# Kernel optimization log

Measured on AMD Instinct MI355X. Metric: run time of the kernel, lower is better.

The kernel has to match this reference:

```python
import jax, jax.numpy as jnp
import numpy as np

N_NODES = 100000
N_EDGES = 600000
IN_C = 128


def setup_inputs() -> dict:
    key = jax.random.key(0)
    ks = jax.random.split(key, 10)
    x = jax.random.normal(ks[0], (N_NODES, IN_C), dtype=jnp.float32)
    edge_index = jax.random.randint(ks[1], (2, N_EDGES), 0, N_NODES, dtype=jnp.int64)
    edge_weight = jax.random.uniform(ks[2], (N_EDGES,), dtype=jnp.float32)
    s = 1.0 / np.sqrt(IN_C)
    # EvolveGCNO initial GCN weight [in, in]
    W0 = jax.random.uniform(ks[3], (IN_C, IN_C), minval=-s, maxval=s, dtype=jnp.float32)
    # GRU(input=in, hidden=in) params, gate order (r, z, n)
    W_ih = jax.random.uniform(ks[4], (3 * IN_C, IN_C), minval=-s, maxval=s, dtype=jnp.float32)
    W_hh = jax.random.uniform(ks[5], (3 * IN_C, IN_C), minval=-s, maxval=s, dtype=jnp.float32)
    b_ih = jax.random.uniform(ks[6], (3 * IN_C,), minval=-s, maxval=s, dtype=jnp.float32)
    b_hh = jax.random.uniform(ks[7], (3 * IN_C,), minval=-s, maxval=s, dtype=jnp.float32)
    cls_w = jax.random.uniform(ks[8], (1, IN_C), minval=-s, maxval=s, dtype=jnp.float32)
    cls_b = jax.random.uniform(ks[9], (1,), minval=-s, maxval=s, dtype=jnp.float32)
    return {"x": x, "edge_index": edge_index, "edge_weight": edge_weight,
            "W0": W0, "W_ih": W_ih, "W_hh": W_hh, "b_ih": b_ih, "b_hh": b_hh,
            "cls_w": cls_w, "cls_b": cls_b}


def reference(x, edge_index, edge_weight, W0, W_ih, W_hh, b_ih, b_hh, cls_w, cls_b):
    n = x.shape[0]
    # --- EvolveGCNO: GRU step with input = hidden = W0 (batch = in_channels rows) ---
    gi = W0 @ W_ih.T + b_ih
    gh = W0 @ W_hh.T + b_hh
    i_r, i_z, i_n = jnp.split(gi, 3, axis=1)
    h_r, h_z, h_n = jnp.split(gh, 3, axis=1)
    r = jax.nn.sigmoid(i_r + h_r)
    z = jax.nn.sigmoid(i_z + h_z)
    cand = jnp.tanh(i_n + r * h_n)
    W = (1.0 - z) * cand + z * W0  # evolved GCN weight [in, in]
    # --- GCNConv with fixed W: add self-loops, symmetric normalization ---
    loops = jnp.arange(n, dtype=edge_index.dtype)
    row = jnp.concatenate([edge_index[0], loops])  # source
    col = jnp.concatenate([edge_index[1], loops])  # target
    w = jnp.concatenate([edge_weight, jnp.ones((n,), x.dtype)])
    deg = jax.ops.segment_sum(w, col, num_segments=n)
    dinv = jnp.where(deg > 0, jax.lax.rsqrt(jnp.maximum(deg, 1e-30)), 0.0)
    norm = dinv[row] * w * dinv[col]  # [E+N]
    h = x @ W  # [N, in]
    agg = jax.ops.segment_sum(norm[:, None] * h[row], col, num_segments=n)  # [N, in]
    # --- ReLU + linear classifier ---
    h = jax.nn.relu(agg)
    return h @ cls_w.T + cls_b  # [N, 1]
```

## Files before the change

kernel.cpp:

```cpp
#include <hip/hip_runtime.h>
#include <math.h>

#define IN_C 128

typedef short short8 __attribute__((ext_vector_type(8)));
typedef float floatx4 __attribute__((ext_vector_type(4)));
typedef unsigned long long u64;

static __device__ __forceinline__ unsigned short f2bf(float f) {
    unsigned int u = __float_as_uint(f);
    u += 0x7fffu + ((u >> 16) & 1u);
    return (unsigned short)(u >> 16);
}

static __device__ __forceinline__ u64 pack_sn(unsigned int src, float norm) {
    return (u64)src | ((u64)__float_as_uint(norm) << 32);
}

__global__ __launch_bounds__(256) void evolve_hist(
        const float* __restrict__ W0, const float* __restrict__ Wih,
        const float* __restrict__ Whh, const float* __restrict__ bih,
        const float* __restrict__ bhh, unsigned short* __restrict__ Wbt,
        const int* __restrict__ coli, const float* __restrict__ ew,
        u64* __restrict__ pk, unsigned int* __restrict__ rank, int E) {
    const int b = blockIdx.x;
    const int t = threadIdx.x;

    if (b < 64) {
        __shared__ float w0row[2][IN_C];
        const int r2 = t >> 7;
        const int j = t & 127;
        const int i = b * 2 + r2;
        w0row[r2][j] = W0[i * IN_C + j];
        __syncthreads();
        float ir = bih[j], iz = bih[j + IN_C], inn = bih[j + 2 * IN_C];
        float hr = bhh[j], hz = bhh[j + IN_C], hnn = bhh[j + 2 * IN_C];
        const float* wr = &Wih[(size_t)j * IN_C];
        const float* wz = &Wih[(size_t)(j + IN_C) * IN_C];
        const float* wn = &Wih[(size_t)(j + 2 * IN_C) * IN_C];
        const float* ur = &Whh[(size_t)j * IN_C];
        const float* uz = &Whh[(size_t)(j + IN_C) * IN_C];
        const float* un = &Whh[(size_t)(j + 2 * IN_C) * IN_C];
        #pragma unroll 4
        for (int k = 0; k < IN_C; ++k) {
            const float a = w0row[r2][k];
            ir = fmaf(a, wr[k], ir); iz = fmaf(a, wz[k], iz); inn = fmaf(a, wn[k], inn);
            hr = fmaf(a, ur[k], hr); hz = fmaf(a, uz[k], hz); hnn = fmaf(a, un[k], hnn);
        }
        const float r = 1.0f / (1.0f + expf(-(ir + hr)));
        const float z = 1.0f / (1.0f + expf(-(iz + hz)));
        const float cand = tanhf(inn + r * hnn);
        Wbt[j * IN_C + i] = f2bf((1.0f - z) * cand + z * w0row[r2][j]);
    } else {
        const int e0 = ((b - 64) * 256 + t) * 4;
        if (e0 + 3 < E) {
            const int4 c4 = *(const int4*)&coli[e0];
            const float4 w4 = *(const float4*)&ew[e0];
            const u64 o0 = atomicAdd(&pk[c4.x], (1ull << 32) | (u64)(unsigned int)(w4.x * 16777216.0f));
            const u64 o1 = atomicAdd(&pk[c4.y], (1ull << 32) | (u64)(unsigned int)(w4.y * 16777216.0f));
            const u64 o2 = atomicAdd(&pk[c4.z], (1ull << 32) | (u64)(unsigned int)(w4.z * 16777216.0f));
            const u64 o3 = atomicAdd(&pk[c4.w], (1ull << 32) | (u64)(unsigned int)(w4.w * 16777216.0f));
            uint4 rk;
            rk.x = (unsigned int)(o0 >> 32); rk.y = (unsigned int)(o1 >> 32);
            rk.z = (unsigned int)(o2 >> 32); rk.w = (unsigned int)(o3 >> 32);
            *(uint4*)&rank[e0] = rk;
        } else {
            for (int e = e0; e < E; ++e) {
                const u64 o = atomicAdd(&pk[coli[e]],
                    (1ull << 32) | (u64)(unsigned int)(ew[e] * 16777216.0f));
                rank[e] = (unsigned int)(o >> 32);
            }
        }
    }
}

__global__ void scan1(const u64* __restrict__ pk, int* __restrict__ rowptr,
                      int* __restrict__ partials, float* __restrict__ dinv, int n) {
    __shared__ int s[256];
    const int t = threadIdx.x;
    const int i = blockIdx.x * 256 + t;
    const u64 pv = (i < n) ? pk[i] : 0ull;
    if (i < n)
        dinv[i] = rsqrtf((float)(unsigned int)(pv & 0xffffffffull) * (1.0f / 16777216.0f) + 1.0f);
    s[t] = (int)(pv >> 32);
    __syncthreads();
    #pragma unroll
    for (int off = 1; off < 256; off <<= 1) {
        const int v = (t >= off) ? s[t - off] : 0;
        __syncthreads();
        s[t] += v;
        __syncthreads();
    }
    if (i < n) rowptr[i] = (t == 0) ? 0 : s[t - 1];
    if (t == 255) partials[blockIdx.x] = s[255];
}

__global__ __launch_bounds__(512) void scan23(int* __restrict__ rowptr,
                                              const int* __restrict__ partials,
                                              int nb, int n, int E) {
    __shared__ int s[512];
    const int t = threadIdx.x;
    const int b = blockIdx.x;
    s[t] = (t < nb) ? partials[t] : 0;
    __syncthreads();
    #pragma unroll
    for (int off = 1; off < 512; off <<= 1) {
        const int v = (t >= off) ? s[t - off] : 0;
        __syncthreads();
        s[t] += v;
        __syncthreads();
    }
    const int add = (b == 0) ? 0 : s[b - 1];
    if (t < 256) {
        const int i = b * 256 + t;
        if (i < n) rowptr[i] += add;
    }
    if (b == 0 && t == 0) rowptr[n] = E;
}

#define ALD 136
__global__ __launch_bounds__(256) void place_gemm(
        const int* __restrict__ rowi, const int* __restrict__ coli,
        const float* __restrict__ ew, const float* __restrict__ dinv,
        const int* __restrict__ rowptr, const unsigned int* __restrict__ rank,
        u64* __restrict__ edge_sn, int E, int PB,
        const float* __restrict__ x, const unsigned short* __restrict__ Wbt,
        unsigned short* __restrict__ hb, int n) {
    __shared__ unsigned short As[128 * ALD];
    __shared__ unsigned short Ws[128 * ALD];
    const int b = blockIdx.x;
    const int t = threadIdx.x;

    if (b < PB) {
        const int e0 = (b * 256 + t) * 4;
        if (e0 + 3 < E) {
            const int4 r4 = *(const int4*)&rowi[e0];
            const int4 c4 = *(const int4*)&coli[e0];
            const float4 w4 = *(const float4*)&ew[e0];
            const uint4 rk = *(const uint4*)&rank[e0];
            __builtin_nontemporal_store(pack_sn((unsigned)r4.x, dinv[r4.x] * w4.x * dinv[c4.x]), &edge_sn[rowptr[c4.x] + rk.x]);
            __builtin_nontemporal_store(pack_sn((unsigned)r4.y, dinv[r4.y] * w4.y * dinv[c4.y]), &edge_sn[rowptr[c4.y] + rk.y]);
            __builtin_nontemporal_store(pack_sn((unsigned)r4.z, dinv[r4.z] * w4.z * dinv[c4.z]), &edge_sn[rowptr[c4.z] + rk.z]);
            __builtin_nontemporal_store(pack_sn((unsigned)r4.w, dinv[r4.w] * w4.w * dinv[c4.w]), &edge_sn[rowptr[c4.w] + rk.w]);
        } else {
            for (int e = e0; e < E; ++e) {
                const int r = rowi[e], c = coli[e];
                edge_sn[rowptr[c] + rank[e]] = pack_sn((unsigned)r, dinv[r] * ew[e] * dinv[c]);
            }
        }
        return;
    }

    const size_t row0 = (size_t)(b - PB) * 128;

    for (int idx = t; idx < 2048; idx += 256) {
        const int nn = idx >> 4, k8 = (idx & 15) * 8;
        *(uint4*)&Ws[nn * ALD + k8] = *(const uint4*)&Wbt[nn * IN_C + k8];
    }
    for (int idx = t; idx < 4096; idx += 256) {
        const int r = idx >> 5, c4 = (idx & 31) * 4;
        size_t row = row0 + r;
        if (row >= (size_t)n) row = (size_t)n - 1;
        const float4 v = *(const float4*)&x[row * IN_C + c4];
        ushort4 bb;
        bb.x = f2bf(v.x); bb.y = f2bf(v.y); bb.z = f2bf(v.z); bb.w = f2bf(v.w);
        *(ushort4*)&As[r * ALD + c4] = bb;
    }
    __syncthreads();

    const int w = t >> 6, lane = t & 63, ln = lane & 15, quad = lane >> 4;
    floatx4 acc[2][8];
    #pragma unroll
    for (int mt = 0; mt < 2; ++mt)
        #pragma unroll
        for (int nt = 0; nt < 8; ++nt)
            acc[mt][nt] = (floatx4){0.f, 0.f, 0.f, 0.f};

    #pragma unroll
    for (int k0 = 0; k0 < 128; k0 += 32) {
        const short8 a0 = *(const short8*)&As[(w * 32 + ln) * ALD + k0 + quad * 8];
        const short8 a1 = *(const short8*)&As[(w * 32 + 16 + ln) * ALD + k0 + quad * 8];
        #pragma unroll
        for (int nt = 0; nt < 8; ++nt) {
            const short8 bb = *(const short8*)&Ws[(nt * 16 + ln) * ALD + k0 + quad * 8];
            acc[0][nt] = __builtin_amdgcn_mfma_f32_16x16x32_bf16(a0, bb, acc[0][nt], 0, 0, 0);
            acc[1][nt] = __builtin_amdgcn_mfma_f32_16x16x32_bf16(a1, bb, acc[1][nt], 0, 0, 0);
        }
    }

    #pragma unroll
    for (int mt = 0; mt < 2; ++mt) {
        #pragma unroll
        for (int reg = 0; reg < 4; ++reg) {
            const size_t row = row0 + w * 32 + mt * 16 + quad * 4 + reg;
            if (row < (size_t)n) {
                #pragma unroll
                for (int nt = 0; nt < 8; ++nt)
                    hb[row * IN_C + nt * 16 + ln] = f2bf(acc[mt][nt][reg]);
            }
        }
    }
}

__global__ __launch_bounds__(256) void gather_classify(
        const unsigned short* __restrict__ hb, const float* __restrict__ dinv,
        const int* __restrict__ rowptr, const u64* __restrict__ edge_sn,
        const float* __restrict__ cls_w, const float* __restrict__ cls_b,
        float* __restrict__ out, int n) {
    const int wid = __builtin_amdgcn_readfirstlane((blockIdx.x * blockDim.x + threadIdx.x) >> 6);
    const int lane = threadIdx.x & 63;
    if (wid >= n) return;

    const float dv = dinv[wid];
    unsigned int hv = *(const unsigned int*)&hb[(size_t)wid * IN_C + 2 * lane];
    float ax = dv * dv * __uint_as_float(hv << 16);
    float ay = dv * dv * __uint_as_float(hv & 0xffff0000u);

    const int e0 = rowptr[wid];
    const int e1 = rowptr[wid + 1];
    const int e1m1 = e1 - 1;
    for (int e = e0; e < e1; e += 8) {
        u64 p[8];
        #pragma unroll
        for (int i = 0; i < 8; ++i) {
            const int idx = (e + i < e1) ? (e + i) : e1m1;
            p[i] = __builtin_nontemporal_load(&edge_sn[idx]);
        }
        unsigned int hr[8];
        #pragma unroll
        for (int i = 0; i < 8; ++i)
            hr[i] = *(const unsigned int*)&hb[(size_t)(unsigned int)(p[i] & 0xffffffffull) * IN_C + 2 * lane];
        #pragma unroll
        for (int i = 0; i < 8; ++i) {
            const float nm = (e + i < e1) ? __uint_as_float((unsigned int)(p[i] >> 32)) : 0.0f;
            ax = fmaf(nm, __uint_as_float(hr[i] << 16), ax);
            ay = fmaf(nm, __uint_as_float(hr[i] & 0xffff0000u), ay);
        }
    }

    const float2 wv = *(const float2*)&cls_w[2 * lane];
    float sum = wv.x * fmaxf(ax, 0.0f) + wv.y * fmaxf(ay, 0.0f);
    #pragma unroll
    for (int off = 32; off > 0; off >>= 1) sum += __shfl_down(sum, off);
    if (lane == 0) out[wid] = sum + cls_b[0];
}

extern "C" void kernel_launch(void* const* d_in, const int* in_sizes, int n_in,
                              void* d_out, int out_size, void* d_ws, size_t ws_size,
                              hipStream_t stream) {
    const float* x    = (const float*)d_in[0];
    const int*   eidx = (const int*)d_in[1];
    const float* ew   = (const float*)d_in[2];
    const float* W0   = (const float*)d_in[3];
    const float* Wih  = (const float*)d_in[4];
    const float* Whh  = (const float*)d_in[5];
    const float* bih  = (const float*)d_in[6];
    const float* bhh  = (const float*)d_in[7];
    const float* clsw = (const float*)d_in[8];
    const float* clsb = (const float*)d_in[9];
    float* out = (float*)d_out;

    const int n = in_sizes[0] / IN_C;
    const int E = in_sizes[2];
    const int* rowi = eidx;
    const int* coli = eidx + E;
    const int NB = (n + 255) / 256;

    int* base = (int*)d_ws;
    u64* pk = (u64*)base;
    float* dinv   = (float*)(base + 2 * (size_t)n);
    int* rowptr   = base + 3 * (size_t)n;
    int* partials = base + 4 * (size_t)n + 4;
    unsigned int* rank = (unsigned int*)(base + 4 * (size_t)n + 516);
    size_t off = 4 * (size_t)n + 516 + (size_t)E;
    u64* edge_sn = (u64*)(base + off);
    unsigned short* Wbt = (unsigned short*)(base + off + 2 * (size_t)E);
    unsigned short* hb  = Wbt + 16384;

    const int EB = (E + 1023) / 1024;
    const int GB = (n + 127) / 128;

    (void)hipMemsetAsync(pk, 0, (size_t)n * 8, stream);
    evolve_hist<<<dim3(64 + EB), dim3(256), 0, stream>>>(W0, Wih, Whh, bih, bhh, Wbt,
                                                         coli, ew, pk, rank, E);
    scan1<<<dim3(NB), dim3(256), 0, stream>>>(pk, rowptr, partials, dinv, n);
    scan23<<<dim3(NB), dim3(512), 0, stream>>>(rowptr, partials, NB, n, E);
    place_gemm<<<dim3(EB + GB), dim3(256), 0, stream>>>(rowi, coli, ew, dinv, rowptr, rank,
                                                        edge_sn, E, EB, x, Wbt, hb, n);
    gather_classify<<<dim3((n + 3) / 4), dim3(256), 0, stream>>>(hb, dinv, rowptr, edge_sn,
                                                                 clsw, clsb, out, n);
}
```

Baseline: 229.0 us.

## Co-schedule histogram atomics with GEMM and fold memset into evolve kernel

The hipMemsetAsync of the degree/count array is replaced by zeroing blocks inside the GRU-evolve kernel. The GEMM that computes h = x·W now runs in the same launch as the edge histogram atomics instead of alongside the placement scatter, with the two kinds of block interleaved proportionally across the grid. The aim is to overlap the latency-bound atomic histogram with the compute-heavy GEMM and to drop one memset launch. The placement step becomes a standalone, lighter kernel. The kernel count stays the same, but the histogram now shares the GPU with GEMM blocks that use a lot of LDS.

```diff
diff --git a/kernel.cpp b/kernel.cpp
--- a/kernel.cpp
+++ b/kernel.cpp
@@ -17,15 +17,13 @@
     return (u64)src | ((u64)__float_as_uint(norm) << 32);
 }
 
-__global__ __launch_bounds__(256) void evolve_hist(
+__global__ __launch_bounds__(256) void zero_evolve(
         const float* __restrict__ W0, const float* __restrict__ Wih,
         const float* __restrict__ Whh, const float* __restrict__ bih,
         const float* __restrict__ bhh, unsigned short* __restrict__ Wbt,
-        const int* __restrict__ coli, const float* __restrict__ ew,
-        u64* __restrict__ pk, unsigned int* __restrict__ rank, int E) {
+        u64* __restrict__ pk, int n, int ZB) {
     const int b = blockIdx.x;
     const int t = threadIdx.x;
-
     if (b < 64) {
         __shared__ float w0row[2][IN_C];
         const int r2 = t >> 7;
@@ -52,7 +50,26 @@
         const float cand = tanhf(inn + r * hnn);
         Wbt[j * IN_C + i] = f2bf((1.0f - z) * cand + z * w0row[r2][j]);
     } else {
-        const int e0 = ((b - 64) * 256 + t) * 4;
+        const int stride = ZB * 256;
+        for (int i = (b - 64) * 256 + t; i < n; i += stride) pk[i] = 0ull;
+    }
+}
+
+#define ALD 136
+__global__ __launch_bounds__(256) void hist_gemm(
+        const int* __restrict__ coli, const float* __restrict__ ew,
+        u64* __restrict__ pk, unsigned int* __restrict__ rank, int E, int EB, int M,
+        const float* __restrict__ x, const unsigned short* __restrict__ Wbt,
+        unsigned short* __restrict__ hb, int n) {
+    __shared__ unsigned short As[128 * ALD];
+    __shared__ unsigned short Ws[128 * ALD];
+    const int i = blockIdx.x;
+    const int t = threadIdx.x;
+    const int prev = (int)(((long long)i * EB) / M);
+    const int next = (int)(((long long)(i + 1) * EB) / M);
+
+    if (next > prev) {
+        const int e0 = (prev * 256 + t) * 4;
         if (e0 + 3 < E) {
             const int4 c4 = *(const int4*)&coli[e0];
             const float4 w4 = *(const float4*)&ew[e0];
@@ -71,6 +88,57 @@
                 rank[e] = (unsigned int)(o >> 32);
             }
         }
+        return;
+    }
+
+    const size_t row0 = (size_t)(i - prev) * 128;
+
+    for (int idx = t; idx < 2048; idx += 256) {
+        const int nn = idx >> 4, k8 = (idx & 15) * 8;
+        *(uint4*)&Ws[nn * ALD + k8] = *(const uint4*)&Wbt[nn * IN_C + k8];
+    }
+    for (int idx = t; idx < 4096; idx += 256) {
+        const int r = idx >> 5, c4 = (idx & 31) * 4;
+        size_t row = row0 + r;
+        if (row >= (size_t)n) row = (size_t)n - 1;
+        const float4 v = *(const float4*)&x[row * IN_C + c4];
+        ushort4 bb;
+        bb.x = f2bf(v.x); bb.y = f2bf(v.y); bb.z = f2bf(v.z); bb.w = f2bf(v.w);
+        *(ushort4*)&As[r * ALD + c4] = bb;
+    }
+    __syncthreads();
+
+    const int w = t >> 6, lane = t & 63, ln = lane & 15, quad = lane >> 4;
+    floatx4 acc[2][8];
+    #pragma unroll
+    for (int mt = 0; mt < 2; ++mt)
+        #pragma unroll
+        for (int nt = 0; nt < 8; ++nt)
+            acc[mt][nt] = (floatx4){0.f, 0.f, 0.f, 0.f};
+
+    #pragma unroll
+    for (int k0 = 0; k0 < 128; k0 += 32) {
+        const short8 a0 = *(const short8*)&As[(w * 32 + ln) * ALD + k0 + quad * 8];
+        const short8 a1 = *(const short8*)&As[(w * 32 + 16 + ln) * ALD + k0 + quad * 8];
+        #pragma unroll
+        for (int nt = 0; nt < 8; ++nt) {
+            const short8 bb = *(const short8*)&Ws[(nt * 16 + ln) * ALD + k0 + quad * 8];
+            acc[0][nt] = __builtin_amdgcn_mfma_f32_16x16x32_bf16(a0, bb, acc[0][nt], 0, 0, 0);
+            acc[1][nt] = __builtin_amdgcn_mfma_f32_16x16x32_bf16(a1, bb, acc[1][nt], 0, 0, 0);
+        }
+    }
+
+    #pragma unroll
+    for (int mt = 0; mt < 2; ++mt) {
+        #pragma unroll
+        for (int reg = 0; reg < 4; ++reg) {
+            const size_t row = row0 + w * 32 + mt * 16 + quad * 4 + reg;
+            if (row < (size_t)n) {
+                #pragma unroll
+                for (int nt = 0; nt < 8; ++nt)
+                    hb[row * IN_C + nt * 16 + ln] = f2bf(acc[mt][nt][reg]);
+            }
+        }
     }
 }
 
@@ -118,86 +186,27 @@
     if (b == 0 && t == 0) rowptr[n] = E;
 }
 
-#define ALD 136
-__global__ __launch_bounds__(256) void place_gemm(
-        const int* __restrict__ rowi, const int* __restrict__ coli,
-        const float* __restrict__ ew, const float* __restrict__ dinv,
-        const int* __restrict__ rowptr, const unsigned int* __restrict__ rank,
-        u64* __restrict__ edge_sn, int E, int PB,
-        const float* __restrict__ x, const unsigned short* __restrict__ Wbt,
-        unsigned short* __restrict__ hb, int n) {
-    __shared__ unsigned short As[128 * ALD];
-    __shared__ unsigned short Ws[128 * ALD];
-    const int b = blockIdx.x;
-    const int t = threadIdx.x;
-
-    if (b < PB) {
-        const int e0 = (b * 256 + t) * 4;
-        if (e0 + 3 < E) {
-            const int4 r4 = *(const int4*)&rowi[e0];
-            const int4 c4 = *(const int4*)&coli[e0];
-            const float4 w4 = *(const float4*)&ew[e0];
-            const uint4 rk = *(const uint4*)&rank[e0];
-            __builtin_nontemporal_store(pack_sn((unsigned)r4.x, dinv[r4.x] * w4.x * dinv[c4.x]), &edge_sn[rowptr[c4.x] + rk.x]);
-            __builtin_nontemporal_store(pack_sn((unsigned)r4.y, dinv[r4.y] * w4.y * dinv[c4.y]), &edge_sn[rowptr[c4.y] + rk.y]);
-            __builtin_nontemporal_store(pack_sn((unsigned)r4.z, dinv[r4.z] * w4.z * dinv[c4.z]), &edge_sn[rowptr[c4.z] + rk.z]);
-            __builtin_nontemporal_store(pack_sn((unsigned)r4.w, dinv[r4.w] * w4.w * dinv[c4.w]), &edge_sn[rowptr[c4.w] + rk.w]);
-        } else {
-            for (int e = e0; e < E; ++e) {
-                const int r = rowi[e], c = coli[e];
-                edge_sn[rowptr[c] + rank[e]] = pack_sn((unsigned)r, dinv[r] * ew[e] * dinv[c]);
-            }
-        }
-        return;
-    }
-
-    const size_t row0 = (size_t)(b - PB) * 128;
-
-    for (int idx = t; idx < 2048; idx += 256) {
-        const int nn = idx >> 4, k8 = (idx & 15) * 8;
-        *(uint4*)&Ws[nn * ALD + k8] = *(const uint4*)&Wbt[nn * IN_C + k8];
-    }
-    for (int idx = t; idx < 4096; idx += 256) {
-        const int r = idx >> 5, c4 = (idx & 31) * 4;
-        size_t row = row0 + r;
-        if (row >= (size_t)n) row = (size_t)n - 1;
-        const float4 v = *(const float4*)&x[row * IN_C + c4];
-        ushort4 bb;
-        bb.x = f2bf(v.x); bb.y = f2bf(v.y); bb.z = f2bf(v.z); bb.w = f2bf(v.w);
-        *(ushort4*)&As[r * ALD + c4] = bb;
-    }
-    __syncthreads();
-
-    const int w = t >> 6, lane = t & 63, ln = lane & 15, quad = lane >> 4;
-    floatx4 acc[2][8];
-    #pragma unroll
-    for (int mt = 0; mt < 2; ++mt)
-        #pragma unroll
-        for (int nt = 0; nt < 8; ++nt)
-            acc[mt][nt] = (floatx4){0.f, 0.f, 0.f, 0.f};
-
-    #pragma unroll
-    for (int k0 = 0; k0 < 128; k0 += 32) {
-        const short8 a0 = *(const short8*)&As[(w * 32 + ln) * ALD + k0 + quad * 8];
-        const short8 a1 = *(const short8*)&As[(w * 32 + 16 + ln) * ALD + k0 + quad * 8];
-        #pragma unroll
-        for (int nt = 0; nt < 8; ++nt) {
-            const short8 bb = *(const short8*)&Ws[(nt * 16 + ln) * ALD + k0 + quad * 8];
-            acc[0][nt] = __builtin_amdgcn_mfma_f32_16x16x32_bf16(a0, bb, acc[0][nt], 0, 0, 0);
-            acc[1][nt] = __builtin_amdgcn_mfma_f32_16x16x32_bf16(a1, bb, acc[1][nt], 0, 0, 0);
-        }
-    }
-
-    #pragma unroll
-    for (int mt = 0; mt < 2; ++mt) {
-        #pragma unroll
-        for (int reg = 0; reg < 4; ++reg) {
-            const size_t row = row0 + w * 32 + mt * 16 + quad * 4 + reg;
-            if (row < (size_t)n) {
-                #pragma unroll
-                for (int nt = 0; nt < 8; ++nt)
-                    hb[row * IN_C + nt * 16 + ln] = f2bf(acc[mt][nt][reg]);
-            }
+__global__ __launch_bounds__(256) void place(const int* __restrict__ rowi,
+                                             const int* __restrict__ coli,
+                                             const float* __restrict__ ew,
+                                             const float* __restrict__ dinv,
+                                             const int* __restrict__ rowptr,
+                                             const unsigned int* __restrict__ rank,
+                                             u64* __restrict__ edge_sn, int E) {
+    const int e0 = (blockIdx.x * 256 + threadIdx.x) * 4;
+    if (e0 + 3 < E) {
+        const int4 r4 = *(const int4*)&rowi[e0];
+        const int4 c4 = *(const int4*)&coli[e0];
+        const float4 w4 = *(const float4*)&ew[e0];
+        const uint4 rk = *(const uint4*)&rank[e0];
+        __builtin_nontemporal_store(pack_sn((unsigned)r4.x, dinv[r4.x] * w4.x * dinv[c4.x]), &edge_sn[rowptr[c4.x] + rk.x]);
+        __builtin_nontemporal_store(pack_sn((unsigned)r4.y, dinv[r4.y] * w4.y * dinv[c4.y]), &edge_sn[rowptr[c4.y] + rk.y]);
+        __builtin_nontemporal_store(pack_sn((unsigned)r4.z, dinv[r4.z] * w4.z * dinv[c4.z]), &edge_sn[rowptr[c4.z] + rk.z]);
+        __builtin_nontemporal_store(pack_sn((unsigned)r4.w, dinv[r4.w] * w4.w * dinv[c4.w]), &edge_sn[rowptr[c4.w] + rk.w]);
+    } else {
+        for (int e = e0; e < E; ++e) {
+            const int r = rowi[e], c = coli[e];
+            edge_sn[rowptr[c] + rank[e]] = pack_sn((unsigned)r, dinv[r] * ew[e] * dinv[c]);
         }
     }
 }
@@ -279,14 +288,14 @@
 
     const int EB = (E + 1023) / 1024;
     const int GB = (n + 127) / 128;
-
-    (void)hipMemsetAsync(pk, 0, (size_t)n * 8, stream);
-    evolve_hist<<<dim3(64 + EB), dim3(256), 0, stream>>>(W0, Wih, Whh, bih, bhh, Wbt,
-                                                         coli, ew, pk, rank, E);
+    const int M = EB + GB;
+    const int ZB = 128;
+
+    zero_evolve<<<dim3(64 + ZB), dim3(256), 0, stream>>>(W0, Wih, Whh, bih, bhh, Wbt, pk, n, ZB);
+    hist_gemm<<<dim3(M), dim3(256), 0, stream>>>(coli, ew, pk, rank, E, EB, M, x, Wbt, hb, n);
     scan1<<<dim3(NB), dim3(256), 0, stream>>>(pk, rowptr, partials, dinv, n);
     scan23<<<dim3(NB), dim3(512), 0, stream>>>(rowptr, partials, NB, n, E);
-    place_gemm<<<dim3(EB + GB), dim3(256), 0, stream>>>(rowi, coli, ew, dinv, rowptr, rank,
-                                                        edge_sn, E, EB, x, Wbt, hb, n);
+    place<<<dim3(EB), dim3(256), 0, stream>>>(rowi, coli, ew, dinv, rowptr, rank, edge_sn, E);
     gather_classify<<<dim3((n + 3) / 4), dim3(256), 0, stream>>>(hb, dinv, rowptr, edge_sn,
                                                                  clsw, clsb, out, n);
 }
```

Measured after the change: 225.7 us. About the same (-1.5%).
